# Performance work log

Hardware: AMD Instinct MI355X
Metric: run time of the kernel (lower is better)

Reference implementation:

```python
import jax, jax.numpy as jnp
import numpy as np

RING_SIZES = list(range(3, 27, 2))  # 3,5,...,25 -> 12 rings; (1+12)*96 = 1248
BN_EPS = 1e-5


def _box_sum(x, k):
    """Sum over k x k window (k odd), 'same' zero padding. x: [B,C,H,W].
    O(1) per pixel via summed-area table instead of dense depthwise conv."""
    p = k // 2
    H, W = x.shape[2], x.shape[3]
    xp = jnp.pad(x, ((0, 0), (0, 0), (p, p), (p, p)))
    S = jnp.cumsum(jnp.cumsum(xp, axis=2), axis=3)
    S = jnp.pad(S, ((0, 0), (0, 0), (1, 0), (1, 0)))  # leading zero row/col
    return (S[:, :, k:k + H, k:k + W] - S[:, :, :H, k:k + W]
            - S[:, :, k:k + H, :W] + S[:, :, :H, :W])


def _ring_sum(x, k):
    """Depthwise conv with a k x k ring of ones == box(k) - box(k-2)."""
    inner = x if k == 3 else _box_sum(x, k - 2)
    return _box_sum(x, k) - inner


def _bn_eval(x, gamma, beta, mean, var):
    scale = gamma / jnp.sqrt(var + BN_EPS)
    return x * scale[None, :, None, None] + (beta - mean * scale)[None, :, None, None]


def _conv1x1(x, w, b):
    # x: [B,C,H,W], w: [O,C] -> [B,O,H,W]
    return jnp.einsum('bchw,oc->bohw', x, w) + b[None, :, None, None]


def setup_inputs() -> dict:
    key = jax.random.key(0)
    ks = jax.random.split(key, 13)
    B, C, H, W = 4, 96, 128, 128
    return {
        'x': jax.random.normal(ks[0], (B, C, H, W), jnp.float32),
        'bn1_gamma': jax.random.uniform(ks[1], (1248,), jnp.float32, 0.5, 1.5),
        'bn1_beta': jax.random.normal(ks[2], (1248,), jnp.float32) * 0.1,
        'bn1_mean': jax.random.normal(ks[3], (1248,), jnp.float32),
        'bn1_var': jax.random.uniform(ks[4], (1248,), jnp.float32, 0.5, 1.5),
        'conv1_w': jax.random.normal(ks[5], (512, 1248), jnp.float32) * (1.0 / np.sqrt(1248)),
        'conv1_b': jax.random.normal(ks[6], (512,), jnp.float32) * 0.01,
        'bn2_gamma': jax.random.uniform(ks[7], (512,), jnp.float32, 0.5, 1.5),
        'bn2_beta': jax.random.normal(ks[8], (512,), jnp.float32) * 0.1,
        'bn2_mean': jax.random.normal(ks[9], (512,), jnp.float32),
        'bn2_var': jax.random.uniform(ks[10], (512,), jnp.float32, 0.5, 1.5),
        'conv2_w': jax.random.normal(ks[11], (96, 512), jnp.float32) * (1.0 / np.sqrt(512)),
        'conv2_b': jax.random.normal(ks[12], (96,), jnp.float32) * 0.01,
    }


def reference(x, bn1_gamma, bn1_beta, bn1_mean, bn1_var, conv1_w, conv1_b,
              bn2_gamma, bn2_beta, bn2_mean, bn2_var, conv2_w, conv2_b):
    convs = [x] + [_ring_sum(x, k) for k in RING_SIZES]
    h = jnp.concatenate(convs, axis=1)  # [B, 1248, H, W]
    h = _bn_eval(h, bn1_gamma, bn1_beta, bn1_mean, bn1_var)
    h = jax.nn.relu(_conv1x1(h, conv1_w, conv1_b))
    h = _bn_eval(h, bn2_gamma, bn2_beta, bn2_mean, bn2_var)
    return _conv1x1(h, conv2_w, conv2_b)
```

## Files before the change

kernel.cpp:

```cpp
#include <hip/hip_runtime.h>
#include <hip/hip_bf16.h>
#include <cstdint>

typedef __attribute__((ext_vector_type(8))) short bf16x8;
typedef __attribute__((ext_vector_type(4))) float f32x4;

#define BN_EPS 1e-5f

__global__ __launch_bounds__(256) void prep1_kernel(
    const float* __restrict__ W1, const float* __restrict__ cb1,
    const float* __restrict__ g1, const float* __restrict__ be1,
    const float* __restrict__ mu1, const float* __restrict__ va1,
    __hip_bfloat16* __restrict__ V, float* __restrict__ b1e)
{
  int o = blockIdx.x;
  int t = threadIdx.x;
  const float* wrow = W1 + (size_t)o * 1248;
  float acc = 0.f;
  for (int i = t; i < 1248; i += 256) {
    float s = g1[i] * rsqrtf(va1[i] + BN_EPS);
    float w = wrow[i];
    acc += w * (be1[i] - mu1[i] * s);
    float g = w * s;
    float gn = 0.f;
    if (i < 1152) {
      float sn = g1[i + 96] * rsqrtf(va1[i + 96] + BN_EPS);
      gn = wrow[i + 96] * sn;
    }
    V[(size_t)o * 1248 + i] = __float2bfloat16(g - gn);
  }
  for (int d = 32; d > 0; d >>= 1) acc += __shfl_down(acc, d);
  __shared__ float red[4];
  int lane = t & 63, wv = t >> 6;
  if (lane == 0) red[wv] = acc;
  __syncthreads();
  if (t == 0) b1e[o] = cb1[o] + red[0] + red[1] + red[2] + red[3];
}

__global__ __launch_bounds__(256) void prep2_kernel(
    const float* __restrict__ W2, const float* __restrict__ cb2,
    const float* __restrict__ g2, const float* __restrict__ be2,
    const float* __restrict__ mu2, const float* __restrict__ va2,
    __hip_bfloat16* __restrict__ W2e, float* __restrict__ b2e)
{
  int o = blockIdx.x;
  int t = threadIdx.x;
  const float* wrow = W2 + (size_t)o * 512;
  float acc = 0.f;
  for (int j = t; j < 512; j += 256) {
    float s = g2[j] * rsqrtf(va2[j] + BN_EPS);
    float wv = wrow[j];
    acc += wv * (be2[j] - mu2[j] * s);
    W2e[(size_t)o * 512 + j] = __float2bfloat16(wv * s);
  }
  for (int d = 32; d > 0; d >>= 1) acc += __shfl_down(acc, d);
  __shared__ float red[4];
  int lane = t & 63, wv2 = t >> 6;
  if (lane == 0) red[wv2] = acc;
  __syncthreads();
  if (t == 0) b2e[o] = cb2[o] + red[0] + red[1] + red[2] + red[3];
}

__global__ __launch_bounds__(128) void sat_kernel(
    const float* __restrict__ x, float* __restrict__ SAT)
{
  int plane = blockIdx.x;
  const float* xp = x + (size_t)plane * 16384;
  __shared__ float tile[16384];
  int t = threadIdx.x;
  for (int i = t; i < 16384; i += 128) {
    int r = i >> 7, c = i & 127;
    tile[r * 128 + (c ^ (r & 31))] = xp[i];
  }
  __syncthreads();
  {
    float run = 0.f;
    int r = t;
    for (int c = 0; c < 128; ++c) {
      int a = r * 128 + (c ^ (r & 31));
      run += tile[a];
      tile[a] = run;
    }
  }
  __syncthreads();
  float* Sg = SAT + (size_t)plane * 17028;
  Sg[t] = 0.f;
  if (t < 4) Sg[128 + t] = 0.f;
  Sg[(t + 1) * 132] = 0.f;
  float run = 0.f;
  for (int r = 0; r < 128; ++r) {
    run += tile[r * 128 + (t ^ (r & 31))];
    Sg[(r + 1) * 132 + t + 1] = run;
  }
}

__global__ __launch_bounds__(512, 2) void fused1_kernel(
    const float* __restrict__ SAT, const __hip_bfloat16* __restrict__ V,
    const float* __restrict__ b1e, __hip_bfloat16* __restrict__ Y1, int nb)
{
  __shared__ __align__(16) float E[96 * 132];
  __shared__ __align__(16) __hip_bfloat16 As[128 * 40];

  int blk = blockIdx.x;
  int rows_per_xcd = (nb * 128) >> 3;
  int r = (blk & 7) * rows_per_xcd + (blk >> 3);
  int bL = r >> 7, y = r & 127;

  int t = threadIdx.x;
  int lane = t & 63, wv = t >> 6;
  int lr = lane & 15, quad = lane >> 4;

  const float* Sb = SAT + (size_t)bL * 96 * 17028;

  int bpx = t & 127;
  int bg = t >> 7;

  f32x4 acc[8][4];
#pragma unroll
  for (int i = 0; i < 8; ++i)
#pragma unroll
    for (int jn = 0; jn < 4; ++jn) acc[i][jn] = (f32x4){0.f, 0.f, 0.f, 0.f};

  auto efill = [&](int j) {
    int y1 = (y - j < 0) ? 0 : (y - j);
    int y2 = ((y + j > 127) ? 127 : (y + j)) + 1;
    for (int idx = t; idx < 3168; idx += 512) {
      int cl = idx / 33;
      int ck = idx - cl * 33;
      const float* bp = Sb + (size_t)cl * 17028 + ck * 4;
      float4 a = *(const float4*)(bp + y2 * 132);
      float4 b = *(const float4*)(bp + y1 * 132);
      float4 d;
      d.x = a.x - b.x; d.y = a.y - b.y; d.z = a.z - b.z; d.w = a.w - b.w;
      *(float4*)(E + cl * 132 + ck * 4) = d;
    }
  };

  int x1 = 0, x2 = 0;
  auto build = [&](int j, int sub) {
    const float* Eb = E + (sub * 32 + bg * 8) * 132;
    union { bf16x8 v; __hip_bfloat16 h[8]; } pk;
#pragma unroll
    for (int i = 0; i < 8; ++i)
      pk.h[i] = __float2bfloat16(Eb[i * 132 + x2] - Eb[i * 132 + x1]);
    *(bf16x8*)(As + bpx * 40 + bg * 8) = pk.v;
  };

  efill(0);
  __syncthreads();

  for (int j = 0; j < 13; ++j) {
    x1 = (bpx - j < 0) ? 0 : (bpx - j);
    x2 = ((bpx + j > 127) ? 127 : (bpx + j)) + 1;
    for (int sub = 0; sub < 3; ++sub) {
      build(j, sub);
      __syncthreads();
      if (sub == 2 && j < 12) efill(j + 1);
      bf16x8 af[8], bfr[4];
#pragma unroll
      for (int i = 0; i < 8; ++i)
        af[i] = *(const bf16x8*)(As + (i * 16 + lr) * 40 + quad * 8);
#pragma unroll
      for (int jn = 0; jn < 4; ++jn)
        bfr[jn] = *(const bf16x8*)(V + (size_t)(wv * 64 + jn * 16 + lr) * 1248
                                   + j * 96 + sub * 32 + quad * 8);
#pragma unroll
      for (int i = 0; i < 8; ++i)
#pragma unroll
        for (int jn = 0; jn < 4; ++jn)
          acc[i][jn] = __builtin_amdgcn_mfma_f32_16x16x32_bf16(af[i], bfr[jn], acc[i][jn], 0, 0, 0);
      __syncthreads();
    }
  }

  size_t mrow = (size_t)bL * 16384 + (size_t)y * 128;
#pragma unroll
  for (int jn = 0; jn < 4; ++jn) {
    int n = wv * 64 + jn * 16 + lr;
    float bias = b1e[n];
#pragma unroll
    for (int i = 0; i < 8; ++i) {
      int pbase = i * 16 + quad * 4;
#pragma unroll
      for (int rr = 0; rr < 4; ++rr) {
        float z = acc[i][jn][rr] + bias;
        z = z > 0.f ? z : 0.f;
        Y1[(mrow + pbase + rr) * 512 + n] = __float2bfloat16(z);
      }
    }
  }
}

__global__ __launch_bounds__(256) void gemm2_kernel(
    const __hip_bfloat16* __restrict__ Y1,
    const __hip_bfloat16* __restrict__ W2e,
    const float* __restrict__ b2e,
    float* __restrict__ out, int b0)
{
  int lane = threadIdx.x & 63, wv = threadIdx.x >> 6;
  int lr = lane & 15, quad = lane >> 4;
  int pw = blockIdx.x * 256 + wv * 64;

  f32x4 acc[6][4];
#pragma unroll
  for (int im = 0; im < 6; ++im)
#pragma unroll
    for (int jn = 0; jn < 4; ++jn) acc[im][jn] = (f32x4){0.f, 0.f, 0.f, 0.f};

  for (int k0 = 0; k0 < 512; k0 += 32) {
    bf16x8 bfrag[4], afrag[6];
#pragma unroll
    for (int jn = 0; jn < 4; ++jn)
      bfrag[jn] = *(const bf16x8*)(Y1 + (size_t)(pw + jn * 16 + lr) * 512 + k0 + quad * 8);
#pragma unroll
    for (int im = 0; im < 6; ++im)
      afrag[im] = *(const bf16x8*)(W2e + (size_t)(im * 16 + lr) * 512 + k0 + quad * 8);
#pragma unroll
    for (int im = 0; im < 6; ++im)
#pragma unroll
      for (int jn = 0; jn < 4; ++jn)
        acc[im][jn] = __builtin_amdgcn_mfma_f32_16x16x32_bf16(afrag[im], bfrag[jn], acc[im][jn], 0, 0, 0);
  }

#pragma unroll
  for (int im = 0; im < 6; ++im) {
#pragma unroll
    for (int r = 0; r < 4; ++r) {
      int o2 = im * 16 + quad * 4 + r;
      float bias = b2e[o2];
#pragma unroll
      for (int jn = 0; jn < 4; ++jn) {
        int p = pw + jn * 16 + lr;
        out[((size_t)(b0 + (p >> 14)) * 96 + o2) * 16384 + (p & 16383)] =
            acc[im][jn][r] + bias;
      }
    }
  }
}

extern "C" void kernel_launch(void* const* d_in, const int* in_sizes, int n_in,
                              void* d_out, int out_size, void* d_ws, size_t ws_size,
                              hipStream_t stream)
{
  const float* x   = (const float*)d_in[0];
  const float* g1  = (const float*)d_in[1];
  const float* be1 = (const float*)d_in[2];
  const float* mu1 = (const float*)d_in[3];
  const float* va1 = (const float*)d_in[4];
  const float* W1  = (const float*)d_in[5];
  const float* cb1 = (const float*)d_in[6];
  const float* g2  = (const float*)d_in[7];
  const float* be2 = (const float*)d_in[8];
  const float* mu2 = (const float*)d_in[9];
  const float* va2 = (const float*)d_in[10];
  const float* W2  = (const float*)d_in[11];
  const float* cb2 = (const float*)d_in[12];
  float* out = (float*)d_out;

  char* w = (char*)d_ws;
  __hip_bfloat16* V   = (__hip_bfloat16*)w; w += (size_t)512 * 1248 * 2;
  __hip_bfloat16* W2e = (__hip_bfloat16*)w; w += (size_t)96 * 512 * 2;
  float* b1e = (float*)w; w += 2048;
  float* b2e = (float*)w; w += 512;
  size_t fixed = (size_t)(w - (char*)d_ws);

  const size_t satB = (size_t)96 * 17028 * 4;
  const size_t yB   = (size_t)16384 * 512 * 2;
  int nb = (ws_size >= fixed + 4 * (satB + yB) + 4096) ? 4 : 1;

  float* SAT = (float*)w; w += (size_t)nb * satB;
  w = (char*)(((uintptr_t)w + 255) & ~(uintptr_t)255);
  __hip_bfloat16* Y1 = (__hip_bfloat16*)w;

  prep1_kernel<<<512, 256, 0, stream>>>(W1, cb1, g1, be1, mu1, va1, V, b1e);
  prep2_kernel<<<96, 256, 0, stream>>>(W2, cb2, g2, be2, mu2, va2, W2e, b2e);

  for (int b0 = 0; b0 < 4; b0 += nb) {
    sat_kernel<<<nb * 96, 128, 0, stream>>>(x + (size_t)b0 * 96 * 16384, SAT);
    fused1_kernel<<<nb * 128, 512, 0, stream>>>(SAT, V, b1e, Y1, nb);
    gemm2_kernel<<<nb * 64, 256, 0, stream>>>(Y1, W2e, b2e, out, b0);
  }
}
```

Baseline: 317.6 us.

## Build full ring A-tile per step, stage Y1 stores through LDS, vectorize SAT

The fused kernel now builds the A operand for all three 32-channel sub-chunks of a ring at once in a wider LDS tile. It then runs the three MFMA sub-steps behind a single barrier and overlaps the next E fill with the first sub-step, cutting syncs from six to two per ring. The Y1 epilogue is staged through shared memory so global writes become coalesced 16-byte stores instead of scattered 2-byte ones. Shared memory moves to a dynamic 77 KB allocation with occupancy hint 4, and the SAT kernel uses float4 loads and scans with a 16-byte-granular swizzle. The larger LDS footprint may limit how many blocks fit per CU.

After: 844.5 us. +165.9%, slower.

```diff
diff --git a/kernel.cpp b/kernel.cpp
--- a/kernel.cpp
+++ b/kernel.cpp
@@ -68,18 +68,23 @@
   const float* xp = x + (size_t)plane * 16384;
   __shared__ float tile[16384];
   int t = threadIdx.x;
-  for (int i = t; i < 16384; i += 128) {
-    int r = i >> 7, c = i & 127;
-    tile[r * 128 + (c ^ (r & 31))] = xp[i];
+  for (int i4 = t; i4 < 4096; i4 += 128) {
+    int r = i4 >> 5;
+    int g = i4 & 31;
+    float4 v = *(const float4*)(xp + (size_t)r * 128 + g * 4);
+    *(float4*)(tile + r * 128 + ((g ^ (r & 31)) << 2)) = v;
   }
   __syncthreads();
   {
-    float run = 0.f;
     int r = t;
-    for (int c = 0; c < 128; ++c) {
-      int a = r * 128 + (c ^ (r & 31));
-      run += tile[a];
-      tile[a] = run;
+    float carry = 0.f;
+    for (int g = 0; g < 32; ++g) {
+      float* p = tile + r * 128 + ((g ^ (r & 31)) << 2);
+      float4 v = *(float4*)p;
+      float s0 = carry + v.x, s1 = s0 + v.y, s2 = s1 + v.z, s3 = s2 + v.w;
+      float4 o; o.x = s0; o.y = s1; o.z = s2; o.w = s3;
+      *(float4*)p = o;
+      carry = s3;
     }
   }
   __syncthreads();
@@ -87,19 +92,21 @@
   Sg[t] = 0.f;
   if (t < 4) Sg[128 + t] = 0.f;
   Sg[(t + 1) * 132] = 0.f;
+  int gc = t >> 2, wc = t & 3;
   float run = 0.f;
   for (int r = 0; r < 128; ++r) {
-    run += tile[r * 128 + (t ^ (r & 31))];
+    run += tile[r * 128 + ((gc ^ (r & 31)) << 2) + wc];
     Sg[(r + 1) * 132 + t + 1] = run;
   }
 }
 
-__global__ __launch_bounds__(512, 2) void fused1_kernel(
+__global__ __launch_bounds__(512, 4) void fused1_kernel(
     const float* __restrict__ SAT, const __hip_bfloat16* __restrict__ V,
     const float* __restrict__ b1e, __hip_bfloat16* __restrict__ Y1, int nb)
 {
-  __shared__ __align__(16) float E[96 * 132];
-  __shared__ __align__(16) __hip_bfloat16 As[128 * 40];
+  extern __shared__ __align__(16) char smem[];
+  float* E = (float*)smem;
+  __hip_bfloat16* As = (__hip_bfloat16*)(smem + 50688);
 
   int blk = blockIdx.x;
   int rows_per_xcd = (nb * 128) >> 3;
@@ -109,11 +116,10 @@
   int t = threadIdx.x;
   int lane = t & 63, wv = t >> 6;
   int lr = lane & 15, quad = lane >> 4;
+  int px = t & 127;
+  int bg = t >> 7;
 
   const float* Sb = SAT + (size_t)bL * 96 * 17028;
-
-  int bpx = t & 127;
-  int bg = t >> 7;
 
   f32x4 acc[8][4];
 #pragma unroll
@@ -136,30 +142,30 @@
     }
   };
 
-  int x1 = 0, x2 = 0;
-  auto build = [&](int j, int sub) {
-    const float* Eb = E + (sub * 32 + bg * 8) * 132;
-    union { bf16x8 v; __hip_bfloat16 h[8]; } pk;
-#pragma unroll
-    for (int i = 0; i < 8; ++i)
-      pk.h[i] = __float2bfloat16(Eb[i * 132 + x2] - Eb[i * 132 + x1]);
-    *(bf16x8*)(As + bpx * 40 + bg * 8) = pk.v;
-  };
-
   efill(0);
   __syncthreads();
 
   for (int j = 0; j < 13; ++j) {
-    x1 = (bpx - j < 0) ? 0 : (bpx - j);
-    x2 = ((bpx + j > 127) ? 127 : (bpx + j)) + 1;
+    int x1 = (px - j < 0) ? 0 : (px - j);
+    int x2 = ((px + j > 127) ? 127 : (px + j)) + 1;
+#pragma unroll
+    for (int pass = 0; pass < 3; ++pass) {
+      int g = bg + pass * 4;
+      const float* Eb = E + g * 8 * 132;
+      union { bf16x8 v; __hip_bfloat16 h[8]; } pk;
+#pragma unroll
+      for (int i = 0; i < 8; ++i)
+        pk.h[i] = __float2bfloat16(Eb[i * 132 + x2] - Eb[i * 132 + x1]);
+      *(bf16x8*)(As + px * 104 + g * 8) = pk.v;
+    }
+    __syncthreads();
+
+#pragma unroll
     for (int sub = 0; sub < 3; ++sub) {
-      build(j, sub);
-      __syncthreads();
-      if (sub == 2 && j < 12) efill(j + 1);
       bf16x8 af[8], bfr[4];
 #pragma unroll
       for (int i = 0; i < 8; ++i)
-        af[i] = *(const bf16x8*)(As + (i * 16 + lr) * 40 + quad * 8);
+        af[i] = *(const bf16x8*)(As + (i * 16 + lr) * 104 + sub * 32 + quad * 8);
 #pragma unroll
       for (int jn = 0; jn < 4; ++jn)
         bfr[jn] = *(const bf16x8*)(V + (size_t)(wv * 64 + jn * 16 + lr) * 1248
@@ -169,25 +175,42 @@
 #pragma unroll
         for (int jn = 0; jn < 4; ++jn)
           acc[i][jn] = __builtin_amdgcn_mfma_f32_16x16x32_bf16(af[i], bfr[jn], acc[i][jn], 0, 0, 0);
-      __syncthreads();
-    }
+      if (sub == 0 && j < 12) efill(j + 1);
+    }
+    __syncthreads();
   }
 
   size_t mrow = (size_t)bL * 16384 + (size_t)y * 128;
-#pragma unroll
-  for (int jn = 0; jn < 4; ++jn) {
-    int n = wv * 64 + jn * 16 + lr;
-    float bias = b1e[n];
-#pragma unroll
-    for (int i = 0; i < 8; ++i) {
-      int pbase = i * 16 + quad * 4;
-#pragma unroll
-      for (int rr = 0; rr < 4; ++rr) {
-        float z = acc[i][jn][rr] + bias;
-        z = z > 0.f ? z : 0.f;
-        Y1[(mrow + pbase + rr) * 512 + n] = __float2bfloat16(z);
+  __hip_bfloat16* Yst = (__hip_bfloat16*)smem;
+#pragma unroll
+  for (int half = 0; half < 2; ++half) {
+    if ((wv >> 2) == half) {
+      __hip_bfloat16* st = Yst + (size_t)(wv & 3) * (128 * 64);
+#pragma unroll
+      for (int jn = 0; jn < 4; ++jn) {
+        int n = wv * 64 + jn * 16 + lr;
+        float bias = b1e[n];
+#pragma unroll
+        for (int i = 0; i < 8; ++i) {
+#pragma unroll
+          for (int rr = 0; rr < 4; ++rr) {
+            int m = i * 16 + quad * 4 + rr;
+            float z = acc[i][jn][rr] + bias;
+            z = z > 0.f ? z : 0.f;
+            st[m * 64 + jn * 16 + lr] = __float2bfloat16(z);
+          }
+        }
       }
     }
+    __syncthreads();
+#pragma unroll
+    for (int it = 0; it < 8; ++it) {
+      int q = it * 512 + t;
+      int p2 = q >> 5, ck = q & 31;
+      uint4 v = *(uint4*)(Yst + (size_t)(ck >> 3) * (128 * 64) + p2 * 64 + (ck & 7) * 8);
+      *(uint4*)(Y1 + (mrow + p2) * 512 + half * 256 + ck * 8) = v;
+    }
+    __syncthreads();
   }
 }
 
@@ -257,6 +280,13 @@
   const float* cb2 = (const float*)d_in[12];
   float* out = (float*)d_out;
 
+  static bool attr_set = false;
+  if (!attr_set) {
+    hipFuncSetAttribute((const void*)fused1_kernel,
+                        hipFuncAttributeMaxDynamicSharedMemorySize, 77312);
+    attr_set = true;
+  }
+
   char* w = (char*)d_ws;
   __hip_bfloat16* V   = (__hip_bfloat16*)w; w += (size_t)512 * 1248 * 2;
   __hip_bfloat16* W2e = (__hip_bfloat16*)w; w += (size_t)96 * 512 * 2;
@@ -277,7 +307,7 @@
 
   for (int b0 = 0; b0 < 4; b0 += nb) {
     sat_kernel<<<nb * 96, 128, 0, stream>>>(x + (size_t)b0 * 96 * 16384, SAT);
-    fused1_kernel<<<nb * 128, 512, 0, stream>>>(SAT, V, b1e, Y1, nb);
+    fused1_kernel<<<nb * 128, 512, 77312, stream>>>(SAT, V, b1e, Y1, nb);
     gemm2_kernel<<<nb * 64, 256, 0, stream>>>(Y1, W2e, b2e, out, b0);
   }
 }
```
